# Performance work log

Hardware: AMD Instinct MI355X
Metric: run time of the kernel (lower is better)

The kernel has to match this reference:

```python
import jax, jax.numpy as jnp
import numpy as np
from jax import lax

NPOINT = 1024
K = 32
EPS = 1e-5  # BatchNorm eps (eval mode, running stats)


def _fps(xyz, npoint):
    """Farthest point sampling. xyz: [B,N,3] -> idx [B,npoint] (int32).
    Deterministic start at index 0 (torch version starts at a random index)."""
    B, N, _ = xyz.shape
    barange = jnp.arange(B)

    def step(carry, _):
        distance, farthest = carry
        centroid = xyz[barange, farthest]                    # [B,3]
        d = jnp.sum((xyz - centroid[:, None, :]) ** 2, -1)   # [B,N]
        distance = jnp.minimum(distance, d)
        new_far = jnp.argmax(distance, axis=-1).astype(jnp.int32)
        return (distance, new_far), farthest

    init = (jnp.full((B, N), 1e10, dtype=xyz.dtype), jnp.zeros((B,), jnp.int32))
    _, centroids = lax.scan(step, init, None, length=npoint)  # [npoint,B]
    return centroids.T                                        # [B,npoint]


def _square_distance(src, dst):
    # src [B,M,3], dst [B,N,3] -> [B,M,N]
    return (jnp.sum(src ** 2, -1)[:, :, None]
            - 2.0 * jnp.einsum('bmc,bnc->bmn', src, dst)
            + jnp.sum(dst ** 2, -1)[:, None, :])


def _gather(p, idx):
    # p [B,N,C], idx [B,...] -> [B,...,C]
    return jax.vmap(lambda pb, ib: pb[ib])(p, idx)


def _mlp_layer(x, w, cb, g, b, m, v):
    # x [B,S,K,Cin]; Conv2d 1x1 == channel matmul, then eval-mode BN, ReLU
    x = jnp.einsum('bskc,oc->bsko', x, w) + cb
    x = (x - m) * (g / jnp.sqrt(v + EPS)) + b
    return jax.nn.relu(x)


def _forward(xyz, points, w0, cb0, g0, b0, m0, v0,
             w1, cb1, g1, b1, m1, v1, w2, cb2, g2, b2, m2, v2):
    fps_idx = _fps(xyz, NPOINT)                       # [B,S]
    new_xyz = _gather(xyz, fps_idx)                   # [B,S,3]
    dists = _square_distance(new_xyz, xyz)            # [B,S,N]
    _, nn_idx = lax.top_k(-dists, K)                  # [B,S,K]
    grouped_xyz = _gather(xyz, nn_idx)                # [B,S,K,3]
    grouped_xyz_norm = grouped_xyz - new_xyz[:, :, None, :]
    grouped_pts = _gather(points, nn_idx)             # [B,S,K,C]
    x = jnp.concatenate([grouped_xyz_norm, grouped_pts], axis=-1)  # [B,S,K,3+C]
    x = _mlp_layer(x, w0, cb0, g0, b0, m0, v0)
    x = _mlp_layer(x, w1, cb1, g1, b1, m1, v1)
    x = _mlp_layer(x, w2, cb2, g2, b2, m2, v2)
    new_points = jnp.max(x, axis=2)                   # max over K -> [B,S,Cout]
    return new_xyz, jnp.transpose(new_points, (0, 2, 1))  # [B,Cout,S]


def setup_inputs() -> dict:
    key = jax.random.key(0)
    ks = jax.random.split(key, 8)
    B, N, C = 16, 4096, 64
    inp = {
        'xyz': jax.random.normal(ks[0], (B, N, 3), jnp.float32),
        'points': jax.random.normal(ks[1], (B, N, C), jnp.float32),
    }
    channels = [(3 + C, 64), (64, 64), (64, 128)]
    for li, (ci, co) in enumerate(channels):
        inp[f'w{li}'] = jax.random.normal(ks[2 + li], (co, ci), jnp.float32) * 0.05
        inp[f'cb{li}'] = jnp.zeros((co,), jnp.float32)
        inp[f'g{li}'] = jnp.ones((co,), jnp.float32)
        inp[f'b{li}'] = jnp.zeros((co,), jnp.float32)
        inp[f'm{li}'] = jnp.zeros((co,), jnp.float32)
        inp[f'v{li}'] = jnp.ones((co,), jnp.float32)
    return inp


def reference(xyz, points, w0, cb0, g0, b0, m0, v0,
              w1, cb1, g1, b1, m1, v1, w2, cb2, g2, b2, m2, v2):
    return _forward(xyz, points, w0, cb0, g0, b0, m0, v0,
                    w1, cb1, g1, b1, m1, v1, w2, cb2, g2, b2, m2, v2)
```

## Files before the change

### kernel.cpp

```cpp
#include <hip/hip_runtime.h>
#include <math.h>

#define NPTS 4096
#define NB 16
#define NS 1024
#define KNB 32
#define CPTS 64

#define WFRAG_ELEMS 18432
#define BIAS_OFF_B  36864
#define FLAG_OFF_B  38912
#define CNT_OFF_B   38976
#define PUBC_OFF_B  39168
#define NGROUPS     2048

typedef __attribute__((ext_vector_type(8))) short short8;
typedef __attribute__((ext_vector_type(4))) float f32x4;

__device__ __forceinline__ short f2bf(float f) {
  unsigned u = __float_as_uint(f);
  unsigned r = (u + 0x7fffu + ((u >> 16) & 1u)) >> 16;
  return (short)r;
}

template <int CTRL>
__device__ __forceinline__ int dppmov(int cur) {
  return __builtin_amdgcn_update_dpp(cur, cur, CTRL, 0xF, 0xF, false);
}
template <int CTRL>
__device__ __forceinline__ void dpp_min_u64(unsigned& hi, unsigned& lo) {
  unsigned nhi = (unsigned)dppmov<CTRL>((int)hi);
  unsigned nlo = (unsigned)dppmov<CTRL>((int)lo);
  bool lt = (nhi < hi) || (nhi == hi && nlo < lo);
  hi = lt ? nhi : hi;
  lo = lt ? nlo : lo;
}
template <int CTRL>
__device__ __forceinline__ void dpp_max_u64(unsigned& hi, unsigned& lo) {
  unsigned nhi = (unsigned)dppmov<CTRL>((int)hi);
  unsigned nlo = (unsigned)dppmov<CTRL>((int)lo);
  bool gt = (nhi > hi) || (nhi == hi && nlo > lo);
  hi = gt ? nhi : hi;
  lo = gt ? nlo : lo;
}

__global__ __launch_bounds__(256) void setup_kernel(
    const float* __restrict__ w0, const float* __restrict__ cb0, const float* __restrict__ g0,
    const float* __restrict__ b0, const float* __restrict__ m0, const float* __restrict__ v0,
    const float* __restrict__ w1, const float* __restrict__ cb1, const float* __restrict__ g1,
    const float* __restrict__ b1, const float* __restrict__ m1, const float* __restrict__ v1,
    const float* __restrict__ w2, const float* __restrict__ cb2, const float* __restrict__ g2,
    const float* __restrict__ b2, const float* __restrict__ m2, const float* __restrict__ v2,
    char* __restrict__ wsb) {
  int i = blockIdx.x * 256 + threadIdx.x;
  short* wf = (short*)wsb;
  float* bias = (float*)(wsb + BIAS_OFF_B);
  if (i < WFRAG_ELEMS) {
    int g = i >> 9, lane = (i >> 3) & 63, j = i & 7;
    int l, nt, s;
    if (g < 12)      { l = 0; nt = g / 3;  s = g % 3; }
    else if (g < 20) { l = 1; int gg = g - 12; nt = gg >> 1; s = gg & 1; }
    else             { l = 2; int gg = g - 20; nt = gg >> 1; s = gg & 1; }
    int n = nt * 16 + (lane & 15);
    int k = s * 32 + ((lane >> 4) << 3) + j;
    float val = 0.f;
    if (l == 0) { if (k < 67) val = w0[n * 67 + k] * (g0[n] / sqrtf(v0[n] + 1e-5f)); }
    else if (l == 1) { val = w1[n * 64 + k] * (g1[n] / sqrtf(v1[n] + 1e-5f)); }
    else { val = w2[n * 64 + k] * (g2[n] / sqrtf(v2[n] + 1e-5f)); }
    wf[i] = f2bf(val);
  } else if (i < WFRAG_ELEMS + 256) {
    int o = i - WFRAG_ELEMS;
    if (o < 64)       { float s = g0[o] / sqrtf(v0[o] + 1e-5f); bias[o] = (cb0[o] - m0[o]) * s + b0[o]; }
    else if (o < 128) { int c = o - 64;  float s = g1[c] / sqrtf(v1[c] + 1e-5f); bias[o] = (cb1[c] - m1[c]) * s + b1[c]; }
    else              { int c = o - 128; float s = g2[c] / sqrtf(v2[c] + 1e-5f); bias[o] = (cb2[c] - m2[c]) * s + b2[c]; }
  } else if (i < WFRAG_ELEMS + 256 + 17) {
    int k = i - (WFRAG_ELEMS + 256);
    if (k < 16) ((unsigned*)(wsb + FLAG_OFF_B))[k] = 0u;
    else        *((unsigned*)(wsb + CNT_OFF_B)) = 0u;
  }
}

#define XSTR 104
__global__ __launch_bounds__(512, 2) void fused_kernel(
    const float* __restrict__ xyz, const float* __restrict__ points,
    char* __restrict__ wsb, float* __restrict__ newxyz, float* __restrict__ outp) {
  struct FpsSh {
    float4 sxyz4[NPTS];
    float4 centL[NS];
    unsigned long long part[2][8];
  };
  struct WorkerSh {
    short Wlds[WFRAG_ELEMS];
    union {
      unsigned long long slist[2][4096];
      short X[8][32 * XSTR];
    } u;
    unsigned long long wl[2][128];
    int nnL[8][KNB];
    float pubq[8][3];
    unsigned gshare;
  };
  __shared__ union { FpsSh f; WorkerSh w; } sh;

  const int t = threadIdx.x;
  const int lane = t & 63;
  const int wave = t >> 6;
  unsigned* flagp = (unsigned*)(wsb + FLAG_OFF_B);
  float* pubC = (float*)(wsb + PUBC_OFF_B);

  if (blockIdx.x < NB) {
    const int b = blockIdx.x;
    const float* xb = xyz + (size_t)b * NPTS * 3;
    float* outb = newxyz + (size_t)b * NS * 3;

    for (int i = t; i < NPTS; i += 512)
      sh.f.sxyz4[i] = make_float4(xb[i * 3 + 0], xb[i * 3 + 1], xb[i * 3 + 2], 0.f);

    float px[8], py[8], pz[8], dist[8];
#pragma unroll
    for (int j = 0; j < 8; ++j) {
      int n = t + 512 * j;
      px[j] = xb[n * 3 + 0];
      py[j] = xb[n * 3 + 1];
      pz[j] = xb[n * 3 + 2];
      dist[j] = 1e10f;
    }
    __syncthreads();
    float cx = sh.f.sxyz4[0].x, cy = sh.f.sxyz4[0].y, cz = sh.f.sxyz4[0].z;
    if (t == 0) sh.f.centL[0] = sh.f.sxyz4[0];

    for (int it = 1; it < NS; ++it) {
      const int buf = it & 1;
      float best = -1.0f; int bidx = 0;
#pragma unroll
      for (int j = 0; j < 8; ++j) {
        float dx = __fsub_rn(px[j], cx);
        float dy = __fsub_rn(py[j], cy);
        float dz = __fsub_rn(pz[j], cz);
        float d  = __fadd_rn(__fadd_rn(__fmul_rn(dx, dx), __fmul_rn(dy, dy)), __fmul_rn(dz, dz));
        float dm = fminf(dist[j], d);
        dist[j] = dm;
        if (dm > best) { best = dm; bidx = t + 512 * j; }
      }
      unsigned hi = __float_as_uint(best);
      unsigned lo = ~(unsigned)bidx;
      dpp_max_u64<0xB1>(hi, lo);
      dpp_max_u64<0x4E>(hi, lo);
      dpp_max_u64<0x141>(hi, lo);
      dpp_max_u64<0x140>(hi, lo);
      dpp_max_u64<0x142>(hi, lo);
      dpp_max_u64<0x143>(hi, lo);
      if (lane == 63) sh.f.part[buf][wave] = ((unsigned long long)hi << 32) | lo;
      __syncthreads();
      unsigned long long k0 = sh.f.part[buf][0];
#pragma unroll
      for (int w = 1; w < 8; ++w) {
        unsigned long long kw = sh.f.part[buf][w];
        k0 = (kw > k0) ? kw : k0;
      }
      int bi = (int)(~(unsigned)k0) & 0xFFFF;
      float4 c4 = sh.f.sxyz4[bi];
      cx = c4.x; cy = c4.y; cz = c4.z;
      if (t == 0) sh.f.centL[it] = c4;
      if ((it & 31) == 31 && wave == 0) {
        if (lane < 32) {
          int ci = it - 31 + lane;
          float4 cc = sh.f.centL[ci];
          float* dst = pubC + ((size_t)b * NS + ci) * 3;
          __hip_atomic_store(dst + 0, cc.x, __ATOMIC_RELAXED, __HIP_MEMORY_SCOPE_AGENT);
          __hip_atomic_store(dst + 1, cc.y, __ATOMIC_RELAXED, __HIP_MEMORY_SCOPE_AGENT);
          __hip_atomic_store(dst + 2, cc.z, __ATOMIC_RELAXED, __HIP_MEMORY_SCOPE_AGENT);
        }
        if (lane == 0)
          __hip_atomic_store(&flagp[b], (unsigned)(it + 1), __ATOMIC_RELEASE, __HIP_MEMORY_SCOPE_AGENT);
      }
    }
    __syncthreads();
    const float* cf = (const float*)sh.f.centL;
    for (int i = t; i < NS * 3; i += 512) {
      int p = i / 3, c = i - p * 3;
      outb[i] = cf[p * 4 + c];
    }
    return;
  }

  {
    const float4* src = (const float4*)wsb;
    float4* dst = (float4*)sh.w.Wlds;
    for (int i = t; i < WFRAG_ELEMS / 8; i += 512) dst[i] = src[i];
  }
  const float* bias = (const float*)(wsb + BIAS_OFF_B);
  unsigned* cntp = (unsigned*)(wsb + CNT_OFF_B);
  const int team = t >> 8, tt = t & 255;

  for (;;) {
    __syncthreads();
    if (t == 0) sh.w.gshare = atomicAdd(cntp, 1u);
    __syncthreads();
    unsigned g = sh.w.gshare;
    if (g >= NGROUPS) break;
    const int b = (int)(g & 15u);
    const int s0 = (int)(g >> 4) << 3;

    if (t == 0) {
      unsigned need = (unsigned)(s0 + 8);
      for (;;) {
        unsigned f = __hip_atomic_load(&flagp[b], __ATOMIC_RELAXED, __HIP_MEMORY_SCOPE_AGENT);
        if (f >= need) break;
        __builtin_amdgcn_s_sleep(8);
      }
    }
    __syncthreads();
    if (t < 24)
      sh.w.pubq[t / 3][t % 3] = __hip_atomic_load(
          &pubC[((size_t)b * NS + s0 + t / 3) * 3 + (t % 3)],
          __ATOMIC_RELAXED, __HIP_MEMORY_SCOPE_AGENT);
    __syncthreads();

    const float* xb = xyz + (size_t)b * NPTS * 3;

    for (int sub = 0; sub < 4; ++sub) {
      const int qi = team * 4 + sub;
      float qx = sh.w.pubq[qi][0], qy = sh.w.pubq[qi][1], qz = sh.w.pubq[qi][2];
      float s2 = __fadd_rn(__fadd_rn(__fmul_rn(qx, qx), __fmul_rn(qy, qy)), __fmul_rn(qz, qz));
      unsigned long long key[16];
#pragma unroll
      for (int j = 0; j < 16; ++j) {
        int n = tt + 256 * j;
        float px = xb[n * 3], py = xb[n * 3 + 1], pz = xb[n * 3 + 2];
        float n2 = __fadd_rn(__fadd_rn(__fmul_rn(px, px), __fmul_rn(py, py)), __fmul_rn(pz, pz));
        float dt = __fadd_rn(__fadd_rn(__fmul_rn(qx, px), __fmul_rn(qy, py)), __fmul_rn(qz, pz));
        float d  = __fadd_rn(__fsub_rn(s2, __fmul_rn(2.0f, dt)), n2);
        unsigned u = __float_as_uint(d);
        u ^= (0x80000000u | (unsigned)((int)u >> 31));
        key[j] = ((unsigned long long)u << 32) | (unsigned)n;
      }
#pragma unroll
      for (int p = 1; p < 16; p <<= 1) {
#pragma unroll
        for (int k = p; k >= 1; k >>= 1) {
#pragma unroll
          for (int j = k % p; j + k < 16; j += 2 * k) {
#pragma unroll
            for (int i = 0; i < k; ++i) {
              if (i + j + k < 16 && (i + j) / (2 * p) == (i + j + k) / (2 * p)) {
                unsigned long long ka = key[i + j], kb = key[i + j + k];
                unsigned long long mn = ka < kb ? ka : kb;
                unsigned long long mx = ka < kb ? kb : ka;
                key[i + j] = mn; key[i + j + k] = mx;
              }
            }
          }
        }
      }
#pragma unroll
      for (int i = 0; i < 16; ++i) sh.w.u.slist[team][i * 256 + tt] = key[i];

      unsigned long long head = key[0];
      unsigned long long nxt  = key[1];
      unsigned p = 1;
      for (int r = 0; r < KNB; ++r) {
        unsigned hi = (unsigned)(head >> 32), lo = (unsigned)head;
        dpp_min_u64<0xB1>(hi, lo);
        dpp_min_u64<0x4E>(hi, lo);
        dpp_min_u64<0x141>(hi, lo);
        dpp_min_u64<0x140>(hi, lo);
        dpp_min_u64<0x142>(hi, lo);
        dpp_min_u64<0x143>(hi, lo);
        unsigned whi = (unsigned)__builtin_amdgcn_readlane((int)hi, 63);
        unsigned wlo = (unsigned)__builtin_amdgcn_readlane((int)lo, 63);
        unsigned long long wkey = ((unsigned long long)whi << 32) | wlo;
        if ((tt & 63) == 0) sh.w.wl[team][(tt >> 6) * 32 + r] = wkey;
        if (head == wkey) {
          head = (p < 16) ? nxt : 0xFFFFFFFFFFFFFFFFull;
          unsigned pn = p + 1;
          nxt = sh.w.u.slist[team][(pn < 16 ? pn : 15) * 256 + tt];
          p = pn;
        }
      }
      __syncthreads();
      if (tt < 128) {
        unsigned long long mykey = sh.w.wl[team][tt];
        int gr = 0;
#pragma unroll 8
        for (int i = 0; i < 128; ++i) gr += (sh.w.wl[team][i] < mykey) ? 1 : 0;
        if (gr < KNB) sh.w.nnL[qi][gr] = (int)(mykey & 0xFFFFFFFFull);
      }
      __syncthreads();
    }

    {
      const int qi = wave;
      const int s = s0 + qi;
      float qx = sh.w.pubq[qi][0], qy = sh.w.pubq[qi][1], qz = sh.w.pubq[qi][2];
      const float* pb = points + (size_t)b * NPTS * CPTS;
      short* X = sh.w.u.X[qi];

      {
        int r = lane & 31, half = lane >> 5;
        int idx = sh.w.nnL[qi][r];
        const float* prow = pb + (size_t)idx * CPTS;
#pragma unroll
        for (int i = 0; i < 48; ++i) {
          int c = half * 48 + i;
          float v;
          if (c < 3) {
            float qc = (c == 0) ? qx : ((c == 1) ? qy : qz);
            v = __fsub_rn(xb[idx * 3 + c], qc);
          } else if (c < 67) {
            v = prow[c - 3];
          } else {
            v = 0.f;
          }
          X[r * XSTR + c] = f2bf(v);
        }
      }

      const int ml = lane & 15, quad = lane >> 4;
      const short8* Wf = (const short8*)sh.w.Wlds;

      short8 a0[2][3];
#pragma unroll
      for (int m2 = 0; m2 < 2; ++m2)
#pragma unroll
        for (int s3 = 0; s3 < 3; ++s3)
          a0[m2][s3] = *(const short8*)&X[(m2 * 16 + ml) * XSTR + s3 * 32 + quad * 8];
      f32x4 acc0[2][4];
#pragma unroll
      for (int m2 = 0; m2 < 2; ++m2)
#pragma unroll
        for (int nt = 0; nt < 4; ++nt) {
          f32x4 c = {0.f, 0.f, 0.f, 0.f};
#pragma unroll
          for (int s3 = 0; s3 < 3; ++s3)
            c = __builtin_amdgcn_mfma_f32_16x16x32_bf16(a0[m2][s3], Wf[(nt * 3 + s3) * 64 + lane], c, 0, 0, 0);
          acc0[m2][nt] = c;
        }
#pragma unroll
      for (int m2 = 0; m2 < 2; ++m2)
#pragma unroll
        for (int nt = 0; nt < 4; ++nt) {
          int ch = nt * 16 + ml;
          float bv = bias[ch];
#pragma unroll
          for (int r4 = 0; r4 < 4; ++r4) {
            float y = fmaxf(acc0[m2][nt][r4] + bv, 0.f);
            int m = quad * 4 + r4;
            int sK = ch >> 5, qq = (ch >> 3) & 3, jj = ch & 7;
            X[((m2 * 2 + sK) * 64 + qq * 16 + m) * 8 + jj] = f2bf(y);
          }
        }

      short8 a1[2][2];
#pragma unroll
      for (int m2 = 0; m2 < 2; ++m2)
#pragma unroll
        for (int sK = 0; sK < 2; ++sK)
          a1[m2][sK] = *(const short8*)&X[((m2 * 2 + sK) * 64 + lane) * 8];
      f32x4 acc1[2][4];
#pragma unroll
      for (int m2 = 0; m2 < 2; ++m2)
#pragma unroll
        for (int nt = 0; nt < 4; ++nt) {
          f32x4 c = {0.f, 0.f, 0.f, 0.f};
#pragma unroll
          for (int sK = 0; sK < 2; ++sK)
            c = __builtin_amdgcn_mfma_f32_16x16x32_bf16(a1[m2][sK], Wf[(12 + nt * 2 + sK) * 64 + lane], c, 0, 0, 0);
          acc1[m2][nt] = c;
        }
#pragma unroll
      for (int m2 = 0; m2 < 2; ++m2)
#pragma unroll
        for (int nt = 0; nt < 4; ++nt) {
          int ch = nt * 16 + ml;
          float bv = bias[64 + ch];
#pragma unroll
          for (int r4 = 0; r4 < 4; ++r4) {
            float y = fmaxf(acc1[m2][nt][r4] + bv, 0.f);
            int m = quad * 4 + r4;
            int sK = ch >> 5, qq = (ch >> 3) & 3, jj = ch & 7;
            X[((m2 * 2 + sK) * 64 + qq * 16 + m) * 8 + jj] = f2bf(y);
          }
        }

      short8 a2[2][2];
#pragma unroll
      for (int m2 = 0; m2 < 2; ++m2)
#pragma unroll
        for (int sK = 0; sK < 2; ++sK)
          a2[m2][sK] = *(const short8*)&X[((m2 * 2 + sK) * 64 + lane) * 8];
#pragma unroll
      for (int nt = 0; nt < 8; ++nt) {
        f32x4 c0 = {0.f, 0.f, 0.f, 0.f}, c1 = {0.f, 0.f, 0.f, 0.f};
        short8 w0f = Wf[(20 + nt * 2 + 0) * 64 + lane];
        short8 w1f = Wf[(20 + nt * 2 + 1) * 64 + lane];
        c0 = __builtin_amdgcn_mfma_f32_16x16x32_bf16(a2[0][0], w0f, c0, 0, 0, 0);
        c0 = __builtin_amdgcn_mfma_f32_16x16x32_bf16(a2[0][1], w1f, c0, 0, 0, 0);
        c1 = __builtin_amdgcn_mfma_f32_16x16x32_bf16(a2[1][0], w0f, c1, 0, 0, 0);
        c1 = __builtin_amdgcn_mfma_f32_16x16x32_bf16(a2[1][1], w1f, c1, 0, 0, 0);
        float bv = bias[128 + nt * 16 + ml];
        float m = -1.f;
#pragma unroll
        for (int r4 = 0; r4 < 4; ++r4) {
          m = fmaxf(m, fmaxf(c0[r4] + bv, 0.f));
          m = fmaxf(m, fmaxf(c1[r4] + bv, 0.f));
        }
        m = fmaxf(m, __shfl_xor(m, 16, 64));
        m = fmaxf(m, __shfl_xor(m, 32, 64));
        if (lane < 16) outp[((size_t)b * 128 + nt * 16 + lane) * NS + s] = m;
      }
    }
  }
}

extern "C" void kernel_launch(void* const* d_in, const int* in_sizes, int n_in,
                              void* d_out, int out_size, void* d_ws, size_t ws_size,
                              hipStream_t stream) {
  const float* xyz    = (const float*)d_in[0];
  const float* points = (const float*)d_in[1];
  const float* w0  = (const float*)d_in[2];
  const float* cb0 = (const float*)d_in[3];
  const float* g0  = (const float*)d_in[4];
  const float* b0  = (const float*)d_in[5];
  const float* m0  = (const float*)d_in[6];
  const float* v0  = (const float*)d_in[7];
  const float* w1  = (const float*)d_in[8];
  const float* cb1 = (const float*)d_in[9];
  const float* g1  = (const float*)d_in[10];
  const float* b1  = (const float*)d_in[11];
  const float* m1  = (const float*)d_in[12];
  const float* v1  = (const float*)d_in[13];
  const float* w2  = (const float*)d_in[14];
  const float* cb2 = (const float*)d_in[15];
  const float* g2  = (const float*)d_in[16];
  const float* b2  = (const float*)d_in[17];
  const float* m2  = (const float*)d_in[18];
  const float* v2  = (const float*)d_in[19];

  char*  wsb    = (char*)d_ws;
  float* newxyz = (float*)d_out;
  float* outp   = (float*)d_out + (size_t)NB * NS * 3;

  setup_kernel<<<(WFRAG_ELEMS + 256 + 17 + 255) / 256, 256, 0, stream>>>(
      w0, cb0, g0, b0, m0, v0, w1, cb1, g1, b1, m1, v1, w2, cb2, g2, b2, m2, v2, wsb);
  fused_kernel<<<256, 512, 0, stream>>>(xyz, points, wsb, newxyz, outp);
}
```

Baseline: 973.4 us.

## Fold setup into fused kernel, split FPS argmax into max then index reduce

The separate setup kernel is removed. Each worker block now builds the bf16 weight fragments and the folded BN bias directly in LDS, and a memset clears the flag and counter words. The FPS argmax reduction is split into a float max across the wave followed by a min-index reduction, instead of a 64-bit packed compare at each DPP step. This shortens the serial per-iteration critical path of farthest point sampling. FPS blocks no longer return when done and join the worker pool afterwards; the progress flag now trails by one batch of 32, which may delay when workers can start.

After: 911.8 us. 6.3% less time.

```diff
diff --git a/kernel.cpp b/kernel.cpp
--- a/kernel.cpp
+++ b/kernel.cpp
@@ -7,11 +7,10 @@
 #define KNB 32
 #define CPTS 64
 
+#define FLAG_OFF_B  0
+#define CNT_OFF_B   64
+#define PUBC_OFF_B  128
 #define WFRAG_ELEMS 18432
-#define BIAS_OFF_B  36864
-#define FLAG_OFF_B  38912
-#define CNT_OFF_B   38976
-#define PUBC_OFF_B  39168
 #define NGROUPS     2048
 
 typedef __attribute__((ext_vector_type(8))) short short8;
@@ -36,53 +35,24 @@
   lo = lt ? nlo : lo;
 }
 template <int CTRL>
-__device__ __forceinline__ void dpp_max_u64(unsigned& hi, unsigned& lo) {
-  unsigned nhi = (unsigned)dppmov<CTRL>((int)hi);
-  unsigned nlo = (unsigned)dppmov<CTRL>((int)lo);
-  bool gt = (nhi > hi) || (nhi == hi && nlo > lo);
-  hi = gt ? nhi : hi;
-  lo = gt ? nlo : lo;
-}
-
-__global__ __launch_bounds__(256) void setup_kernel(
+__device__ __forceinline__ void dpp_fmax(float& m) {
+  m = fmaxf(m, __int_as_float(dppmov<CTRL>(__float_as_int(m))));
+}
+template <int CTRL>
+__device__ __forceinline__ void dpp_umin(unsigned& v) {
+  unsigned o = (unsigned)dppmov<CTRL>((int)v);
+  v = (o < v) ? o : v;
+}
+
+#define XSTR 104
+__global__ __launch_bounds__(512, 2) void fused_kernel(
+    const float* __restrict__ xyz, const float* __restrict__ points,
     const float* __restrict__ w0, const float* __restrict__ cb0, const float* __restrict__ g0,
     const float* __restrict__ b0, const float* __restrict__ m0, const float* __restrict__ v0,
     const float* __restrict__ w1, const float* __restrict__ cb1, const float* __restrict__ g1,
     const float* __restrict__ b1, const float* __restrict__ m1, const float* __restrict__ v1,
     const float* __restrict__ w2, const float* __restrict__ cb2, const float* __restrict__ g2,
     const float* __restrict__ b2, const float* __restrict__ m2, const float* __restrict__ v2,
-    char* __restrict__ wsb) {
-  int i = blockIdx.x * 256 + threadIdx.x;
-  short* wf = (short*)wsb;
-  float* bias = (float*)(wsb + BIAS_OFF_B);
-  if (i < WFRAG_ELEMS) {
-    int g = i >> 9, lane = (i >> 3) & 63, j = i & 7;
-    int l, nt, s;
-    if (g < 12)      { l = 0; nt = g / 3;  s = g % 3; }
-    else if (g < 20) { l = 1; int gg = g - 12; nt = gg >> 1; s = gg & 1; }
-    else             { l = 2; int gg = g - 20; nt = gg >> 1; s = gg & 1; }
-    int n = nt * 16 + (lane & 15);
-    int k = s * 32 + ((lane >> 4) << 3) + j;
-    float val = 0.f;
-    if (l == 0) { if (k < 67) val = w0[n * 67 + k] * (g0[n] / sqrtf(v0[n] + 1e-5f)); }
-    else if (l == 1) { val = w1[n * 64 + k] * (g1[n] / sqrtf(v1[n] + 1e-5f)); }
-    else { val = w2[n * 64 + k] * (g2[n] / sqrtf(v2[n] + 1e-5f)); }
-    wf[i] = f2bf(val);
-  } else if (i < WFRAG_ELEMS + 256) {
-    int o = i - WFRAG_ELEMS;
-    if (o < 64)       { float s = g0[o] / sqrtf(v0[o] + 1e-5f); bias[o] = (cb0[o] - m0[o]) * s + b0[o]; }
-    else if (o < 128) { int c = o - 64;  float s = g1[c] / sqrtf(v1[c] + 1e-5f); bias[o] = (cb1[c] - m1[c]) * s + b1[c]; }
-    else              { int c = o - 128; float s = g2[c] / sqrtf(v2[c] + 1e-5f); bias[o] = (cb2[c] - m2[c]) * s + b2[c]; }
-  } else if (i < WFRAG_ELEMS + 256 + 17) {
-    int k = i - (WFRAG_ELEMS + 256);
-    if (k < 16) ((unsigned*)(wsb + FLAG_OFF_B))[k] = 0u;
-    else        *((unsigned*)(wsb + CNT_OFF_B)) = 0u;
-  }
-}
-
-#define XSTR 104
-__global__ __launch_bounds__(512, 2) void fused_kernel(
-    const float* __restrict__ xyz, const float* __restrict__ points,
     char* __restrict__ wsb, float* __restrict__ newxyz, float* __restrict__ outp) {
   struct FpsSh {
     float4 sxyz4[NPTS];
@@ -97,6 +67,7 @@
     } u;
     unsigned long long wl[2][128];
     int nnL[8][KNB];
+    float biasL[256];
     float pubq[8][3];
     unsigned gshare;
   };
@@ -106,6 +77,7 @@
   const int lane = t & 63;
   const int wave = t >> 6;
   unsigned* flagp = (unsigned*)(wsb + FLAG_OFF_B);
+  unsigned* cntp  = (unsigned*)(wsb + CNT_OFF_B);
   float* pubC = (float*)(wsb + PUBC_OFF_B);
 
   if (blockIdx.x < NB) {
@@ -131,26 +103,29 @@
 
     for (int it = 1; it < NS; ++it) {
       const int buf = it & 1;
-      float best = -1.0f; int bidx = 0;
+      float dm[8];
 #pragma unroll
       for (int j = 0; j < 8; ++j) {
         float dx = __fsub_rn(px[j], cx);
         float dy = __fsub_rn(py[j], cy);
         float dz = __fsub_rn(pz[j], cz);
         float d  = __fadd_rn(__fadd_rn(__fmul_rn(dx, dx), __fmul_rn(dy, dy)), __fmul_rn(dz, dz));
-        float dm = fminf(dist[j], d);
-        dist[j] = dm;
-        if (dm > best) { best = dm; bidx = t + 512 * j; }
-      }
-      unsigned hi = __float_as_uint(best);
-      unsigned lo = ~(unsigned)bidx;
-      dpp_max_u64<0xB1>(hi, lo);
-      dpp_max_u64<0x4E>(hi, lo);
-      dpp_max_u64<0x141>(hi, lo);
-      dpp_max_u64<0x140>(hi, lo);
-      dpp_max_u64<0x142>(hi, lo);
-      dpp_max_u64<0x143>(hi, lo);
-      if (lane == 63) sh.f.part[buf][wave] = ((unsigned long long)hi << 32) | lo;
+        float v  = fminf(dist[j], d);
+        dist[j] = v;
+        dm[j] = v;
+      }
+      float m = fmaxf(fmaxf(fmaxf(dm[0], dm[1]), fmaxf(dm[2], dm[3])),
+                      fmaxf(fmaxf(dm[4], dm[5]), fmaxf(dm[6], dm[7])));
+      dpp_fmax<0xB1>(m);  dpp_fmax<0x4E>(m);  dpp_fmax<0x141>(m);
+      dpp_fmax<0x140>(m); dpp_fmax<0x142>(m); dpp_fmax<0x143>(m);
+      float M = __int_as_float(__builtin_amdgcn_readlane(__float_as_int(m), 63));
+      unsigned idxl = 0xFFFFFFFFu;
+#pragma unroll
+      for (int j = 7; j >= 0; --j) idxl = (dm[j] == M) ? (unsigned)(t + 512 * j) : idxl;
+      dpp_umin<0xB1>(idxl);  dpp_umin<0x4E>(idxl);  dpp_umin<0x141>(idxl);
+      dpp_umin<0x140>(idxl); dpp_umin<0x142>(idxl); dpp_umin<0x143>(idxl);
+      if (lane == 63)
+        sh.f.part[buf][wave] = ((unsigned long long)__float_as_uint(M) << 32) | (unsigned)(~idxl);
       __syncthreads();
       unsigned long long k0 = sh.f.part[buf][0];
 #pragma unroll
@@ -158,11 +133,13 @@
         unsigned long long kw = sh.f.part[buf][w];
         k0 = (kw > k0) ? kw : k0;
       }
-      int bi = (int)(~(unsigned)k0) & 0xFFFF;
+      int bi = (int)(~(unsigned)k0) & 4095;
       float4 c4 = sh.f.sxyz4[bi];
       cx = c4.x; cy = c4.y; cz = c4.z;
       if (t == 0) sh.f.centL[it] = c4;
       if ((it & 31) == 31 && wave == 0) {
+        if (lane == 0)
+          __hip_atomic_store(&flagp[b], (unsigned)(it - 31), __ATOMIC_RELEASE, __HIP_MEMORY_SCOPE_AGENT);
         if (lane < 32) {
           int ci = it - 31 + lane;
           float4 cc = sh.f.centL[ci];
@@ -171,26 +148,41 @@
           __hip_atomic_store(dst + 1, cc.y, __ATOMIC_RELAXED, __HIP_MEMORY_SCOPE_AGENT);
           __hip_atomic_store(dst + 2, cc.z, __ATOMIC_RELAXED, __HIP_MEMORY_SCOPE_AGENT);
         }
-        if (lane == 0)
-          __hip_atomic_store(&flagp[b], (unsigned)(it + 1), __ATOMIC_RELEASE, __HIP_MEMORY_SCOPE_AGENT);
-      }
-    }
+      }
+    }
+    if (wave == 0 && lane == 0)
+      __hip_atomic_store(&flagp[b], (unsigned)NS, __ATOMIC_RELEASE, __HIP_MEMORY_SCOPE_AGENT);
     __syncthreads();
     const float* cf = (const float*)sh.f.centL;
     for (int i = t; i < NS * 3; i += 512) {
       int p = i / 3, c = i - p * 3;
       outb[i] = cf[p * 4 + c];
     }
-    return;
   }
 
-  {
-    const float4* src = (const float4*)wsb;
-    float4* dst = (float4*)sh.w.Wlds;
-    for (int i = t; i < WFRAG_ELEMS / 8; i += 512) dst[i] = src[i];
+  __syncthreads();
+  for (int i = t; i < WFRAG_ELEMS; i += 512) {
+    int g = i >> 9, ln = (i >> 3) & 63, j = i & 7;
+    int l, nt, s;
+    if (g < 12)      { l = 0; nt = g / 3;  s = g % 3; }
+    else if (g < 20) { l = 1; int gg = g - 12; nt = gg >> 1; s = gg & 1; }
+    else             { l = 2; int gg = g - 20; nt = gg >> 1; s = gg & 1; }
+    int n = nt * 16 + (ln & 15);
+    int k = s * 32 + ((ln >> 4) << 3) + j;
+    float val = 0.f;
+    if (l == 0) { if (k < 67) val = w0[n * 67 + k] * (g0[n] / sqrtf(v0[n] + 1e-5f)); }
+    else if (l == 1) { val = w1[n * 64 + k] * (g1[n] / sqrtf(v1[n] + 1e-5f)); }
+    else { val = w2[n * 64 + k] * (g2[n] / sqrtf(v2[n] + 1e-5f)); }
+    sh.w.Wlds[i] = f2bf(val);
   }
-  const float* bias = (const float*)(wsb + BIAS_OFF_B);
-  unsigned* cntp = (unsigned*)(wsb + CNT_OFF_B);
+  if (t < 256) {
+    int o = t;
+    float bv;
+    if (o < 64)       { float sc = g0[o] / sqrtf(v0[o] + 1e-5f); bv = (cb0[o] - m0[o]) * sc + b0[o]; }
+    else if (o < 128) { int c = o - 64;  float sc = g1[c] / sqrtf(v1[c] + 1e-5f); bv = (cb1[c] - m1[c]) * sc + b1[c]; }
+    else              { int c = o - 128; float sc = g2[c] / sqrtf(v2[c] + 1e-5f); bv = (cb2[c] - m2[c]) * sc + b2[c]; }
+    sh.w.biasL[o] = bv;
+  }
   const int team = t >> 8, tt = t & 255;
 
   for (;;) {
@@ -205,7 +197,7 @@
     if (t == 0) {
       unsigned need = (unsigned)(s0 + 8);
       for (;;) {
-        unsigned f = __hip_atomic_load(&flagp[b], __ATOMIC_RELAXED, __HIP_MEMORY_SCOPE_AGENT);
+        unsigned f = __hip_atomic_load(&flagp[b], __ATOMIC_ACQUIRE, __HIP_MEMORY_SCOPE_AGENT);
         if (f >= need) break;
         __builtin_amdgcn_s_sleep(8);
       }
@@ -294,6 +286,7 @@
       const int s = s0 + qi;
       float qx = sh.w.pubq[qi][0], qy = sh.w.pubq[qi][1], qz = sh.w.pubq[qi][2];
       const float* pb = points + (size_t)b * NPTS * CPTS;
+      const float* bias = sh.w.biasL;
       short* X = sh.w.u.X[qi];
 
       {
@@ -441,7 +434,8 @@
   float* newxyz = (float*)d_out;
   float* outp   = (float*)d_out + (size_t)NB * NS * 3;
 
-  setup_kernel<<<(WFRAG_ELEMS + 256 + 17 + 255) / 256, 256, 0, stream>>>(
-      w0, cb0, g0, b0, m0, v0, w1, cb1, g1, b1, m1, v1, w2, cb2, g2, b2, m2, v2, wsb);
-  fused_kernel<<<256, 512, 0, stream>>>(xyz, points, wsb, newxyz, outp);
-}
+  hipMemsetAsync(wsb, 0, 128, stream);
+  fused_kernel<<<256, 512, 0, stream>>>(
+      xyz, points, w0, cb0, g0, b0, m0, v0, w1, cb1, g1, b1, m1, v1,
+      w2, cb2, g2, b2, m2, v2, wsb, newxyz, outp);
+}
```
